# Kernel optimization log

Measured on AMD Instinct MI355X. Metric: run time of the kernel, lower is better.

Reference implementation:

```python
import jax, jax.numpy as jnp
import numpy as np

K = 3  # neighbor_count


def setup_inputs() -> dict:
    key = jax.random.key(0)
    k1, k2, k3, k4, k5 = jax.random.split(key, 5)
    N, M, D = 200000, 64, 256
    node_features = jax.random.normal(k1, (N, D), dtype=jnp.float32)
    neighbors = jax.random.randint(k2, (N, M), 0, N, dtype=jnp.int64)
    # valid neighbor counts; clamp to >= K so every node has a full top-k
    neighbor_counts = jnp.maximum(
        jax.random.randint(k3, (N,), 0, M, dtype=jnp.int64), K)
    W = jax.random.normal(k4, (2 * D,), dtype=jnp.float32) * 0.05
    b = jax.random.normal(k5, (1,), dtype=jnp.float32) * 0.05
    return {"node_features": node_features, "neighbors": neighbors,
            "neighbor_counts": neighbor_counts, "W": W, "b": b}


def reference(node_features, neighbors, neighbor_counts, W, b):
    # fc([x_i ; x_j]) = x_i . W[:D] + x_j . W[D:] + b  (Linear(2D, 1))
    D = node_features.shape[1]
    wa, wb = W[:D], W[D:]
    s_self = node_features @ wa + b[0]          # [N]
    s_all = node_features @ wb                  # [N]
    s_nb = s_all[neighbors]                     # [N, M] gather
    scores = jnp.exp(jax.nn.leaky_relu(s_self[:, None] + s_nb))  # [N, M]
    valid = jnp.arange(neighbors.shape[1])[None, :] < neighbor_counts[:, None]
    scores = jnp.where(valid, scores, -jnp.inf)
    top_vals, top_idx = jax.lax.top_k(scores, K)              # [N, K]
    selected = jnp.take_along_axis(neighbors, top_idx, axis=1)  # [N, K] node ids
    return top_vals, selected
```

## Files before the change

### kernel.cpp

```cpp
#include <hip/hip_runtime.h>
#include <cstdint>

#define D_DIM 256
#define M_DIM 64
#define K_TOP 3

typedef unsigned long long u64;
typedef int   v4i __attribute__((ext_vector_type(4)));
typedef float v4f __attribute__((ext_vector_type(4)));

__global__ __launch_bounds__(256) void ns_scores_kernel(
    const float* __restrict__ nf,
    const float* __restrict__ W,
    const float* __restrict__ b,
    float* __restrict__ s_self,
    float* __restrict__ s_all,
    int N)
{
    const int wave = (blockIdx.x * blockDim.x + threadIdx.x) >> 6;
    const int lane = threadIdx.x & 63;
    const int sub  = lane >> 4;
    const int p    = lane & 15;
    const int row  = wave * 4 + sub;
    if (row >= N) return;

    const v4f* __restrict__ vrow = (const v4f*)(nf + (size_t)row * D_DIM);
    const v4f* __restrict__ wa4  = (const v4f*)W;
    const v4f* __restrict__ wb4  = (const v4f*)(W + D_DIM);

    float sa = 0.0f, sb = 0.0f;
    #pragma unroll
    for (int i = 0; i < 4; ++i) {
        const int o = i * 16 + p;
        const v4f v = vrow[o];
        const v4f a = wa4[o];
        const v4f c = wb4[o];
        sa += v.x * a.x + v.y * a.y + v.z * a.z + v.w * a.w;
        sb += v.x * c.x + v.y * c.y + v.z * c.z + v.w * c.w;
    }
    #pragma unroll
    for (int off = 8; off > 0; off >>= 1) {
        sa += __shfl_xor(sa, off);
        sb += __shfl_xor(sb, off);
    }
    if (p == 0) {
        s_self[row] = sa + b[0];
        s_all[row]  = sb;
    }
}

__global__ __launch_bounds__(256) void ns_topk_kernel(
    const int* __restrict__ neighbors,
    const int* __restrict__ counts,
    const float* __restrict__ s_self,
    const float* __restrict__ s_all,
    float* __restrict__ out_vals,
    float* __restrict__ out_idx,
    int N)
{
    const int wave = (blockIdx.x * blockDim.x + threadIdx.x) >> 6;
    const int lane = threadIdx.x & 63;
    const int sub  = lane >> 4;
    const int p    = lane & 15;
    const int row  = wave * 4 + sub;
    if (row >= N) return;

    const int   cnt = counts[row];
    const float ss  = s_self[row];

    v4i nb = (v4i){0, 0, 0, 0};
    if (p * 4 < cnt) {
        nb = __builtin_nontemporal_load(
            (const v4i*)(neighbors + (size_t)row * M_DIM) + p);
    }

    const int nbs[4] = { nb.x, nb.y, nb.z, nb.w };
    u64 key[4];
    #pragma unroll
    for (int e = 0; e < 4; ++e) {
        const int j = p * 4 + e;
        float score = 0.0f;
        if (j < cnt) {
            const float x  = ss + s_all[nbs[e]];
            const float lr = (x >= 0.0f) ? x : 0.01f * x;
            score = expf(lr);
        }
        key[e] = ((u64)__float_as_uint(score) << 32) | (u64)(63 - j);
    }

    float vals[K_TOP];
    int   idxs[K_TOP];

    #pragma unroll
    for (int k = 0; k < K_TOP; ++k) {
        u64 m = key[0];
        if (key[1] > m) m = key[1];
        if (key[2] > m) m = key[2];
        if (key[3] > m) m = key[3];
        #pragma unroll
        for (int off = 8; off > 0; off >>= 1) {
            const u64 o = __shfl_xor(m, off);
            if (o > m) m = o;
        }
        const int jwin = 63 - (int)(m & 0x3F);
        vals[k] = __uint_as_float((unsigned)(m >> 32));

        const int ew = jwin & 3;
        const int pw = jwin >> 2;
        const int cand = (ew == 0) ? nbs[0] : (ew == 1) ? nbs[1]
                       : (ew == 2) ? nbs[2] : nbs[3];
        idxs[k] = __shfl(cand, (sub << 4) | pw);

        if (p == pw) {
            const u64 dead = (u64)(63 - jwin);
            if      (ew == 0) key[0] = dead;
            else if (ew == 1) key[1] = dead;
            else if (ew == 2) key[2] = dead;
            else              key[3] = dead;
        }
    }

    if (p == 0) {
        const size_t base = (size_t)row * K_TOP;
        #pragma unroll
        for (int k = 0; k < K_TOP; ++k) {
            out_vals[base + k] = vals[k];
            out_idx [base + k] = (float)idxs[k];
        }
    }
}

extern "C" void kernel_launch(void* const* d_in, const int* in_sizes, int n_in,
                              void* d_out, int out_size, void* d_ws, size_t ws_size,
                              hipStream_t stream)
{
    const float* nf        = (const float*)d_in[0];
    const int*   neighbors = (const int*)  d_in[1];
    const int*   counts    = (const int*)  d_in[2];
    const float* W         = (const float*)d_in[3];
    const float* b         = (const float*)d_in[4];

    const int N = in_sizes[2];

    float* s_self = (float*)d_ws;
    float* s_all  = s_self + N;

    float* out_vals = (float*)d_out;
    float* out_idx  = out_vals + (size_t)N * K_TOP;

    const int threads = 256;
    const int rowsPerBlock = (threads / 64) * 4;
    const int blocks = (N + rowsPerBlock - 1) / rowsPerBlock;

    ns_scores_kernel<<<blocks, threads, 0, stream>>>(nf, W, b, s_self, s_all, N);
    ns_topk_kernel<<<blocks, threads, 0, stream>>>(neighbors, counts, s_self, s_all,
                                                   out_vals, out_idx, N);
}
```

Measured before the change: 336.9 us.

## Fuse score and top-k kernels into persistent kernel with grid barrier

Merges the per-node score computation and the neighbor top-k selection into one persistent kernel sized to full occupancy, separated by an atomic software grid barrier. Weight vectors are hoisted into registers and feature loads use nontemporal hints. This aims to remove the second kernel launch and its inter-kernel gap. In exchange it adds a barrier-init launch and spin-wait, reduces the grid size (which may hurt latency hiding for the random gather), and needs an extra workspace word.

```diff
diff --git a/kernel.cpp b/kernel.cpp
--- a/kernel.cpp
+++ b/kernel.cpp
@@ -9,62 +9,12 @@
 typedef int   v4i __attribute__((ext_vector_type(4)));
 typedef float v4f __attribute__((ext_vector_type(4)));
 
-__global__ __launch_bounds__(256) void ns_scores_kernel(
-    const float* __restrict__ nf,
-    const float* __restrict__ W,
-    const float* __restrict__ b,
-    float* __restrict__ s_self,
-    float* __restrict__ s_all,
-    int N)
-{
-    const int wave = (blockIdx.x * blockDim.x + threadIdx.x) >> 6;
-    const int lane = threadIdx.x & 63;
-    const int sub  = lane >> 4;
-    const int p    = lane & 15;
-    const int row  = wave * 4 + sub;
-    if (row >= N) return;
-
-    const v4f* __restrict__ vrow = (const v4f*)(nf + (size_t)row * D_DIM);
-    const v4f* __restrict__ wa4  = (const v4f*)W;
-    const v4f* __restrict__ wb4  = (const v4f*)(W + D_DIM);
-
-    float sa = 0.0f, sb = 0.0f;
-    #pragma unroll
-    for (int i = 0; i < 4; ++i) {
-        const int o = i * 16 + p;
-        const v4f v = vrow[o];
-        const v4f a = wa4[o];
-        const v4f c = wb4[o];
-        sa += v.x * a.x + v.y * a.y + v.z * a.z + v.w * a.w;
-        sb += v.x * c.x + v.y * c.y + v.z * c.z + v.w * c.w;
-    }
-    #pragma unroll
-    for (int off = 8; off > 0; off >>= 1) {
-        sa += __shfl_xor(sa, off);
-        sb += __shfl_xor(sb, off);
-    }
-    if (p == 0) {
-        s_self[row] = sa + b[0];
-        s_all[row]  = sb;
-    }
-}
-
-__global__ __launch_bounds__(256) void ns_topk_kernel(
-    const int* __restrict__ neighbors,
-    const int* __restrict__ counts,
-    const float* __restrict__ s_self,
-    const float* __restrict__ s_all,
-    float* __restrict__ out_vals,
-    float* __restrict__ out_idx,
-    int N)
-{
-    const int wave = (blockIdx.x * blockDim.x + threadIdx.x) >> 6;
-    const int lane = threadIdx.x & 63;
-    const int sub  = lane >> 4;
-    const int p    = lane & 15;
-    const int row  = wave * 4 + sub;
-    if (row >= N) return;
-
+__device__ __forceinline__ void topk_row(
+    const int* __restrict__ neighbors, const int* __restrict__ counts,
+    const float* __restrict__ s_self,  const float* __restrict__ s_all,
+    float* __restrict__ out_vals,      float* __restrict__ out_idx,
+    int row, int sub, int p)
+{
     const int   cnt = counts[row];
     const float ss  = s_self[row];
 
@@ -130,6 +80,137 @@
     }
 }
 
+__global__ void ns_bar_init(unsigned* __restrict__ bar) { *bar = 0u; }
+
+__global__ __launch_bounds__(256) void ns_fused_sw(
+    const float* __restrict__ nf,
+    const int*   __restrict__ neighbors,
+    const int*   __restrict__ counts,
+    const float* __restrict__ W,
+    const float* __restrict__ b,
+    float* __restrict__ s_self,
+    float* __restrict__ s_all,
+    unsigned* __restrict__ bar,
+    float* __restrict__ out_vals,
+    float* __restrict__ out_idx,
+    int N)
+{
+    const int lane = threadIdx.x & 63;
+    const int sub  = lane >> 4;
+    const int p    = lane & 15;
+    const int wid  = (int)((blockIdx.x * blockDim.x + threadIdx.x) >> 6);
+    const int nw   = (int)((gridDim.x * blockDim.x) >> 6);
+    const int nGroups = (N + 3) >> 2;
+
+    const v4f* __restrict__ wa4 = (const v4f*)W;
+    const v4f* __restrict__ wb4 = (const v4f*)(W + D_DIM);
+    v4f wa_r[4], wb_r[4];
+    #pragma unroll
+    for (int i = 0; i < 4; ++i) {
+        wa_r[i] = wa4[i * 16 + p];
+        wb_r[i] = wb4[i * 16 + p];
+    }
+    const float bias = b[0];
+
+    for (int g = wid; g < nGroups; g += nw) {
+        const int row = g * 4 + sub;
+        if (row < N) {
+            const v4f* __restrict__ vrow = (const v4f*)(nf + (size_t)row * D_DIM);
+            float sa = 0.0f, sb = 0.0f;
+            #pragma unroll
+            for (int i = 0; i < 4; ++i) {
+                const v4f v = __builtin_nontemporal_load(vrow + (i * 16 + p));
+                sa += v.x * wa_r[i].x + v.y * wa_r[i].y
+                    + v.z * wa_r[i].z + v.w * wa_r[i].w;
+                sb += v.x * wb_r[i].x + v.y * wb_r[i].y
+                    + v.z * wb_r[i].z + v.w * wb_r[i].w;
+            }
+            #pragma unroll
+            for (int off = 8; off > 0; off >>= 1) {
+                sa += __shfl_xor(sa, off);
+                sb += __shfl_xor(sb, off);
+            }
+            if (p == 0) {
+                s_self[row] = sa + bias;
+                s_all[row]  = sb;
+            }
+        }
+    }
+
+    __syncthreads();
+    if (threadIdx.x == 0) {
+        __threadfence();
+        __hip_atomic_fetch_add(bar, 1u, __ATOMIC_ACQ_REL,
+                               __HIP_MEMORY_SCOPE_AGENT);
+        const unsigned target = gridDim.x;
+        while (__hip_atomic_load(bar, __ATOMIC_ACQUIRE,
+                                 __HIP_MEMORY_SCOPE_AGENT) < target) {
+            __builtin_amdgcn_s_sleep(8);
+        }
+        __threadfence();
+    }
+    __syncthreads();
+
+    for (int g = wid; g < nGroups; g += nw) {
+        const int row = g * 4 + sub;
+        if (row < N) {
+            topk_row(neighbors, counts, s_self, s_all, out_vals, out_idx,
+                     row, sub, p);
+        }
+    }
+}
+
+__global__ __launch_bounds__(256) void ns_scores_kernel(
+    const float* __restrict__ nf, const float* __restrict__ W,
+    const float* __restrict__ b,  float* __restrict__ s_self,
+    float* __restrict__ s_all, int N)
+{
+    const int wave = (blockIdx.x * blockDim.x + threadIdx.x) >> 6;
+    const int lane = threadIdx.x & 63;
+    const int sub  = lane >> 4;
+    const int p    = lane & 15;
+    const int row  = wave * 4 + sub;
+    if (row >= N) return;
+
+    const v4f* __restrict__ vrow = (const v4f*)(nf + (size_t)row * D_DIM);
+    const v4f* __restrict__ wa4  = (const v4f*)W;
+    const v4f* __restrict__ wb4  = (const v4f*)(W + D_DIM);
+
+    float sa = 0.0f, sb = 0.0f;
+    #pragma unroll
+    for (int i = 0; i < 4; ++i) {
+        const int o = i * 16 + p;
+        const v4f v = vrow[o];
+        const v4f a = wa4[o];
+        const v4f c = wb4[o];
+        sa += v.x * a.x + v.y * a.y + v.z * a.z + v.w * a.w;
+        sb += v.x * c.x + v.y * c.y + v.z * c.z + v.w * c.w;
+    }
+    #pragma unroll
+    for (int off = 8; off > 0; off >>= 1) {
+        sa += __shfl_xor(sa, off);
+        sb += __shfl_xor(sb, off);
+    }
+    if (p == 0) {
+        s_self[row] = sa + b[0];
+        s_all[row]  = sb;
+    }
+}
+
+__global__ __launch_bounds__(256) void ns_topk_kernel(
+    const int* __restrict__ neighbors, const int* __restrict__ counts,
+    const float* __restrict__ s_self,  const float* __restrict__ s_all,
+    float* __restrict__ out_vals,      float* __restrict__ out_idx, int N)
+{
+    const int wave = (blockIdx.x * blockDim.x + threadIdx.x) >> 6;
+    const int lane = threadIdx.x & 63;
+    const int sub  = lane >> 4;
+    const int p    = lane & 15;
+    const int row  = wave * 4 + sub;
+    if (row >= N) return;
+    topk_row(neighbors, counts, s_self, s_all, out_vals, out_idx, row, sub, p);
+}
+
 extern "C" void kernel_launch(void* const* d_in, const int* in_sizes, int n_in,
                               void* d_out, int out_size, void* d_ws, size_t ws_size,
                               hipStream_t stream)
@@ -142,17 +223,46 @@
 
     const int N = in_sizes[2];
 
-    float* s_self = (float*)d_ws;
-    float* s_all  = s_self + N;
+    float*    s_self = (float*)d_ws;
+    float*    s_all  = s_self + N;
+    unsigned* bar    = (unsigned*)(s_all + N);
 
     float* out_vals = (float*)d_out;
     float* out_idx  = out_vals + (size_t)N * K_TOP;
 
     const int threads = 256;
     const int rowsPerBlock = (threads / 64) * 4;
-    const int blocks = (N + rowsPerBlock - 1) / rowsPerBlock;
-
-    ns_scores_kernel<<<blocks, threads, 0, stream>>>(nf, W, b, s_self, s_all, N);
-    ns_topk_kernel<<<blocks, threads, 0, stream>>>(neighbors, counts, s_self, s_all,
-                                                   out_vals, out_idx, N);
-}
+    const int needBlocks = (N + rowsPerBlock - 1) / rowsPerBlock;
+
+    static int fusedBlocksMax = 0;
+    if (fusedBlocksMax == 0) {
+        int bpc = 0, dev = 0;
+        hipDeviceProp_t prop;
+        hipError_t e1 = hipOccupancyMaxActiveBlocksPerMultiprocessor(
+            &bpc, ns_fused_sw, threads, 0);
+        hipError_t e2 = hipGetDevice(&dev);
+        hipError_t e3 = hipGetDeviceProperties(&prop, dev);
+        if (e1 == hipSuccess && e2 == hipSuccess && e3 == hipSuccess &&
+            bpc >= 1 && prop.multiProcessorCount >= 1) {
+            fusedBlocksMax = bpc * prop.multiProcessorCount;
+        } else {
+            (void)hipGetLastError();
+            fusedBlocksMax = -1;
+        }
+    }
+
+    if (fusedBlocksMax > 0) {
+        const int blocks = needBlocks < fusedBlocksMax ? needBlocks
+                                                       : fusedBlocksMax;
+        ns_bar_init<<<1, 1, 0, stream>>>(bar);
+        ns_fused_sw<<<blocks, threads, 0, stream>>>(
+            nf, neighbors, counts, W, b, s_self, s_all, bar,
+            out_vals, out_idx, N);
+    } else {
+        ns_scores_kernel<<<needBlocks, threads, 0, stream>>>(nf, W, b,
+                                                             s_self, s_all, N);
+        ns_topk_kernel<<<needBlocks, threads, 0, stream>>>(neighbors, counts,
+                                                           s_self, s_all,
+                                                           out_vals, out_idx, N);
+    }
+}
```

Result: slower. 427.9 us (+27.0%).
